# Kernel optimization log

Measured on AMD Instinct MI355X. Metric: run time of the kernel, lower is better.

Reference implementation:

```python
import jax, jax.numpy as jnp
import numpy as np
from jax import lax

B, S, V, E, H, NH = 32, 512, 30000, 300, 200, 4
ENC = 2 * H           # bidirectional encoder size = 400
DH = ENC // NH        # head dim = 100
BUDGET = 20.0         # percent of length kept by sparseMAP
SCALING = 1.0 / 0.001 # eval-mode temperature (module sets 0.001 at test time)
NEG = -1e9


def setup_inputs():
    key = jax.random.key(0)
    ks = jax.random.split(key, 16)
    lengths = jax.random.randint(ks[0], (B,), S // 2, S + 1)
    mask = jnp.arange(S)[None, :] < lengths[:, None]          # prefix mask [B,S]
    x = jax.random.randint(ks[1], (B, S), 0, V)
    p = lambda k, sh: jax.random.normal(k, sh, jnp.float32) * 0.05
    return {
        "x": x, "mask": mask,
        "embed_table": p(ks[2], (V, E)),
        "w_ih_f": p(ks[3], (4 * H, E)), "w_hh_f": p(ks[4], (4 * H, H)), "b_f": jnp.zeros((4 * H,), jnp.float32),
        "w_ih_b": p(ks[5], (4 * H, E)), "w_hh_b": p(ks[6], (4 * H, H)), "b_b": jnp.zeros((4 * H,), jnp.float32),
        "q_state": p(ks[7], (ENC,)),
        "W_q": p(ks[8], (ENC, ENC)), "W_k": p(ks[9], (ENC, ENC)), "W_v": p(ks[10], (ENC, ENC)),
        "W_out": p(ks[11], (ENC, ENC)),
        "W_head": p(ks[12], (ENC, 1)), "b_head": jnp.zeros((1,), jnp.float32),
    }


def _lstm(xW, mask, W_hh):
    """Masked (packed-equivalent) LSTM. xW: [B,S,4H] precomputed input proj, mask [B,S] bool."""
    Bb, Ss, H4 = xW.shape
    Hh = H4 // 4
    def step(carry, t_in):
        h, c = carry
        g, m = t_in                             # g [B,4H], m [B,1] bool
        gates = g + h @ W_hh.T
        i, f, gg, o = jnp.split(gates, 4, axis=-1)
        c_new = jax.nn.sigmoid(f) * c + jax.nn.sigmoid(i) * jnp.tanh(gg)
        h_new = jax.nn.sigmoid(o) * jnp.tanh(c_new)
        return (jnp.where(m, h_new, h), jnp.where(m, c_new, c)), jnp.where(m, h_new, 0.0)
    init = (jnp.zeros((Bb, Hh), xW.dtype), jnp.zeros((Bb, Hh), xW.dtype))
    xs = (jnp.swapaxes(xW, 0, 1), jnp.swapaxes(mask[..., None], 0, 1))
    _, outs = lax.scan(step, init, xs)
    return jnp.swapaxes(outs, 0, 1)


def _proj_capped_simplex(theta, k):
    """SparseMAP budget QP: argmin ||mu - theta||^2 s.t. 0<=mu<=1, sum(mu)=k.
    Bisection on threshold tau (non-diff), then exact differentiable tau on the free set."""
    th = lax.stop_gradient(theta)
    lo = jnp.min(th) - 1.0
    hi = jnp.max(th)
    def body(_, ab):
        lo, hi = ab
        mid = 0.5 * (lo + hi)
        too_big = jnp.sum(jnp.clip(th - mid, 0.0, 1.0)) > k
        return (jnp.where(too_big, mid, lo), jnp.where(too_big, hi, mid))
    lo, hi = lax.fori_loop(0, 60, body, (lo, hi))
    tau0 = 0.5 * (lo + hi)
    mu0 = th - tau0
    free = (mu0 > 0.0) & (mu0 < 1.0)
    nU = jnp.sum(mu0 >= 1.0).astype(theta.dtype)
    nS = jnp.sum(free).astype(theta.dtype)
    tau = (jnp.sum(jnp.where(free, theta, 0.0)) + nU - k) / jnp.maximum(nS, 1.0)
    tau = jnp.where(nS > 0, tau, tau0)
    return jnp.clip(theta - tau, 0.0, 1.0)


def _forward(x, mask, embed_table, w_ih_f, w_hh_f, b_f, w_ih_b, w_hh_b, b_b,
             q_state, W_q, W_k, W_v, W_out, W_head, b_head):
    lengths = mask.sum(1)                                   # [B] int
    emb = embed_table[x]                                    # [B,S,E] (dropout off: eval)
    # forward direction
    h_f = _lstm(emb @ w_ih_f.T + b_f, mask, w_hh_f)         # [B,S,H]
    # backward direction: reverse each sample within its length (packed semantics)
    t = jnp.arange(S)
    idx = jnp.clip(lengths[:, None] - 1 - t[None, :], 0, S - 1)   # [B,S], involution on valid part
    emb_rev = jnp.take_along_axis(emb, idx[..., None], axis=1)
    h_b_rev = _lstm(emb_rev @ w_ih_b.T + b_b, mask, w_hh_b)
    h_b = jnp.take_along_axis(h_b_rev, idx[..., None], axis=1)
    h_b = jnp.where(mask[..., None], h_b, 0.0)
    h = jnp.concatenate([h_f, h_b], axis=-1)                # [B,S,ENC]
    # Hopfield pooling with learned query state, per-sample sparseMAP top-k budget
    q = (q_state @ W_q).reshape(NH, DH)                     # learned pooling query
    K = (h @ W_k).reshape(B, S, NH, DH)
    Vv = (h @ W_v).reshape(B, S, NH, DH)
    scores = SCALING * jnp.einsum('hd,bshd->bhs', q, K)     # [B,NH,S]
    scores = jnp.where(mask[:, None, :], scores, NEG)
    kbud = jnp.round(BUDGET / 100.0 * lengths.astype(jnp.float32))   # per-sample budget
    proj = jax.vmap(jax.vmap(_proj_capped_simplex, (0, None)), (0, 0))
    p = proj(scores, kbud)                                  # [B,NH,S] sparse marginals
    pooled = jnp.einsum('bhs,bshd->bhd', p, Vv).reshape(B, ENC) @ W_out
    y = jax.nn.sigmoid(pooled @ W_head + b_head)            # [B,1]
    z = jnp.where(mask, p.mean(1), 0.0)                     # [B,S] rationale
    return y, z


def reference(x, mask, embed_table, w_ih_f, w_hh_f, b_f, w_ih_b, w_hh_b, b_b,
              q_state, W_q, W_k, W_v, W_out, W_head, b_head):
    return _forward(x, mask, embed_table, w_ih_f, w_hh_f, b_f, w_ih_b, w_hh_b, b_b,
                    q_state, W_q, W_k, W_v, W_out, W_head, b_head)
```

## Files before the change

kernel.cpp:

```cpp
#include <hip/hip_runtime.h>
#include <hip/hip_bf16.h>
#include <math.h>

#define B_   32
#define S_   512
#define V_   30000
#define E_   300
#define H_   200
#define NH_  4
#define ENC_ 400
#define G4_  800
#define NEGV  (-1e9f)
#define SCALE_ 1000.0f

typedef _Float16 half2v __attribute__((ext_vector_type(2)));
typedef _Float16 f16x8  __attribute__((ext_vector_type(8)));
typedef float    f32x4  __attribute__((ext_vector_type(4)));

#if defined(__has_builtin)
#if __has_builtin(__builtin_amdgcn_fdot2)
#define FDOT2(a,b,c) __builtin_amdgcn_fdot2((a),(b),(c),false)
#endif
#endif
#ifndef FDOT2
#define FDOT2(a,b,c) fmaf((float)(a)[1],(float)(b)[1], fmaf((float)(a)[0],(float)(b)[0],(c)))
#endif

#define OF_QVEC  320000ull
#define OF_WKQ   320448ull
#define OF_THETA 322048ull
#define OF_MU    387584ull
#define OF_HP    453120ull
#define OF_LEN   504320ull
#define OF_XWF   504384ull
#define OF_XWB   13611584ull
#define OF_HF    26718784ull
#define OF_HB    29995584ull

__global__ void k_lengths(const void* __restrict__ mask, int* __restrict__ lengths) {
  int b = blockIdx.x, lane = threadIdx.x;
  const unsigned char* mb = (const unsigned char*)mask;
  int mode;
  if (mb[1] != 0) mode = 0;
  else if (((const int*)mask)[1] != 0) mode = 1;
  else mode = 2;
  int cnt = 0;
  for (int s = lane; s < S_; s += 64) {
    int v;
    if (mode == 0)      v = mb[b*S_ + s] ? 1 : 0;
    else if (mode == 1) v = ((const int*)mask)[b*S_ + s] ? 1 : 0;
    else                v = ((const long long*)mask)[b*S_ + s] ? 1 : 0;
    cnt += v;
  }
  for (int off = 32; off; off >>= 1) cnt += __shfl_xor(cnt, off);
  if (lane == 0) lengths[b] = cnt;
}

__global__ void k_qvec(const float* __restrict__ qs, const float* __restrict__ Wq,
                       float* __restrict__ qvec) {
  __shared__ float qsl[ENC_];
  int t = threadIdx.x;
  if (t < ENC_) qsl[t] = qs[t];
  __syncthreads();
  if (t < ENC_) {
    float acc = 0.f;
    for (int i = 0; i < ENC_; ++i) acc += qsl[i] * Wq[(size_t)i*ENC_ + t];
    qvec[t] = acc;
  }
}

__global__ void k_wkq(const float* __restrict__ Wk, const float* __restrict__ qvec,
                      float* __restrict__ wkq) {
  int t = threadIdx.x;
  int e = blockIdx.x*64 + (t >> 2);
  int head = t & 3;
  if (e < ENC_) {
    float acc = 0.f;
    const float* row = Wk + (size_t)e*ENC_ + head*100;
    const float* qv  = qvec + head*100;
    for (int d = 0; d < 100; ++d) acc += row[d]*qv[d];
    wkq[e*4 + head] = acc;
  }
}

__global__ __launch_bounds__(256) void k_gemm_mfma(
    const int* __restrict__ x, const float* __restrict__ emb,
    const float* __restrict__ wf, const float* __restrict__ wb,
    const float* __restrict__ bf, const float* __restrict__ bb,
    float* __restrict__ xWf, float* __restrict__ xWb)
{
  __shared__ int xid[128];
  __shared__ __align__(16) _Float16 sA[128][40];
  __shared__ __align__(16) _Float16 sB[64][40];
  const int t = threadIdx.x;
  const int row0 = blockIdx.x * 128;
  const int col0 = blockIdx.y * 64;
  if (t < 128) xid[t] = x[row0 + t];
  const int w = t >> 6, lane = t & 63;
  const int wr = w >> 1, wc = w & 1;
  f32x4 acc[4][2] = {};
  const int ar = t >> 1, ah = t & 1;
  const int bc = t >> 2, bq = t & 3;
  const int colg = col0 + bc;
  const float* wsrc = (colg < 800) ? (wf + (size_t)colg*300)
                                   : (wb + (size_t)(colg-800)*300);
  __syncthreads();
  const float* asrc = emb + (size_t)xid[ar]*300;
  for (int kc = 0; kc < 10; ++kc) {
    const int k0 = kc*32;
    {
      const int kb = k0 + ah*16;
      _Float16 tmp[16];
      if (kb + 15 < 300) {
        #pragma unroll
        for (int q = 0; q < 4; ++q) {
          float4 a = *(const float4*)(asrc + kb + 4*q);
          tmp[4*q]  =(_Float16)a.x; tmp[4*q+1]=(_Float16)a.y;
          tmp[4*q+2]=(_Float16)a.z; tmp[4*q+3]=(_Float16)a.w;
        }
      } else {
        #pragma unroll
        for (int i = 0; i < 16; ++i)
          tmp[i] = (_Float16)((kb+i < 300) ? asrc[kb+i] : 0.f);
      }
      *(f16x8*)&sA[ar][ah*16]   = *(f16x8*)&tmp[0];
      *(f16x8*)&sA[ar][ah*16+8] = *(f16x8*)&tmp[8];
    }
    {
      const int kb = k0 + bq*8;
      _Float16 tmp[8];
      if (kb + 7 < 300) {
        #pragma unroll
        for (int q = 0; q < 2; ++q) {
          float4 a = *(const float4*)(wsrc + kb + 4*q);
          tmp[4*q]  =(_Float16)a.x; tmp[4*q+1]=(_Float16)a.y;
          tmp[4*q+2]=(_Float16)a.z; tmp[4*q+3]=(_Float16)a.w;
        }
      } else {
        #pragma unroll
        for (int i = 0; i < 8; ++i)
          tmp[i] = (_Float16)((kb+i < 300) ? wsrc[kb+i] : 0.f);
      }
      *(f16x8*)&sB[bc][bq*8] = *(f16x8*)&tmp[0];
    }
    __syncthreads();
    const int fr = lane & 15, kg = lane >> 4;
    f16x8 b0 = *(const f16x8*)&sB[wc*32 + fr][kg*8];
    f16x8 b1 = *(const f16x8*)&sB[wc*32 + 16 + fr][kg*8];
    #pragma unroll
    for (int m = 0; m < 4; ++m) {
      f16x8 afrag = *(const f16x8*)&sA[wr*64 + m*16 + fr][kg*8];
      acc[m][0] = __builtin_amdgcn_mfma_f32_16x16x32_f16(afrag, b0, acc[m][0], 0,0,0);
      acc[m][1] = __builtin_amdgcn_mfma_f32_16x16x32_f16(afrag, b1, acc[m][1], 0,0,0);
    }
    __syncthreads();
  }
  const int crb = (lane >> 4) * 4, ccol = lane & 15;
  #pragma unroll
  for (int n = 0; n < 2; ++n) {
    int colg2 = col0 + wc*32 + n*16 + ccol;
    bool isF = colg2 < 800;
    int colo = isF ? colg2 : colg2 - 800;
    float bias = isF ? bf[colo] : bb[colo];
    float* dst = isF ? xWf : xWb;
    #pragma unroll
    for (int m = 0; m < 4; ++m) {
      int row = row0 + wr*64 + m*16 + crb;
      #pragma unroll
      for (int r = 0; r < 4; ++r)
        dst[(size_t)(row+r)*800 + colo] = acc[m][n][r] + bias;
    }
  }
}

__global__ __launch_bounds__(1024) void k_lstm_v2(
    const float* __restrict__ xWf, const float* __restrict__ xWb,
    const float* __restrict__ whhf, const float* __restrict__ whhb,
    const int* __restrict__ lengths,
    float* __restrict__ h_f, float* __restrict__ h_b)
{
  const int bid = blockIdx.x;
  const int dir = bid >> 5, b = bid & 31;
  const float* __restrict__ xW  = dir ? xWb : xWf;
  const float* __restrict__ whh = dir ? whhb : whhf;
  float* __restrict__ hout      = dir ? h_b : h_f;
  const int len = lengths[b];
  const int t = threadIdx.x;
  const int active = (t < G4_);

  __shared__ __align__(16) _Float16 hbh[200];
  __shared__ float gact[G4_];

  half2v w[100];
  if (active) {
    const float* rp = whh + (size_t)t*H_;
    #pragma unroll
    for (int j = 0; j < 50; ++j) {
      float2 a = *(const float2*)(rp + 2*j);
      w[j] = half2v{(_Float16)a.x, (_Float16)a.y};
    }
    #pragma unroll
    for (int j = 0; j < 50; ++j) {
      float2 a = *(const float2*)(rp + 100 + 2*j);
      w[50+j] = half2v{(_Float16)a.x, (_Float16)a.y};
    }
  }
  if (t < 200) hbh[t] = (_Float16)0.f;
  float cst = 0.f;
  const float* xbase = xW + (size_t)b*S_*G4_;
  const int isTanh = (t >= 400) && (t < 600);
  __syncthreads();

  for (int step = 0; step < len; ++step) {
    const int pos = dir ? (len-1-step) : step;
    if (active) {
      float xv = xbase[(size_t)pos*G4_ + t];
      float a0 = 0.f, a1 = 0.f;
      #pragma unroll
      for (int j = 0; j < 12; ++j) {
        float4 h4 = *(const float4*)&hbh[8*j];
        a0 = FDOT2(w[4*j],   __builtin_bit_cast(half2v, h4.x), a0);
        a1 = FDOT2(w[4*j+1], __builtin_bit_cast(half2v, h4.y), a1);
        a0 = FDOT2(w[4*j+2], __builtin_bit_cast(half2v, h4.z), a0);
        a1 = FDOT2(w[4*j+3], __builtin_bit_cast(half2v, h4.w), a1);
      }
      {
        float2 h2 = *(const float2*)&hbh[96];
        a0 = FDOT2(w[48], __builtin_bit_cast(half2v, h2.x), a0);
        a1 = FDOT2(w[49], __builtin_bit_cast(half2v, h2.y), a1);
      }
      #pragma unroll
      for (int j = 0; j < 12; ++j) {
        float4 h4 = *(const float4*)&hbh[100 + 8*j];
        a0 = FDOT2(w[50+4*j],   __builtin_bit_cast(half2v, h4.x), a0);
        a1 = FDOT2(w[50+4*j+1], __builtin_bit_cast(half2v, h4.y), a1);
        a0 = FDOT2(w[50+4*j+2], __builtin_bit_cast(half2v, h4.z), a0);
        a1 = FDOT2(w[50+4*j+3], __builtin_bit_cast(half2v, h4.w), a1);
      }
      {
        float2 h2 = *(const float2*)&hbh[196];
        a0 = FDOT2(w[98], __builtin_bit_cast(half2v, h2.x), a0);
        a1 = FDOT2(w[99], __builtin_bit_cast(half2v, h2.y), a1);
      }
      float pre = a0 + a1 + xv;
      float act;
      if (isTanh) {
        float gc = fminf(fmaxf(pre, -10.f), 10.f);
        float e2 = __expf(2.f*gc);
        act = (e2-1.f)/(e2+1.f);
      } else {
        act = 1.f/(1.f+__expf(-pre));
      }
      gact[t] = act;
    }
    __syncthreads();
    if (t < 200) {
      float ig = gact[t], fg = gact[200+t], gg = gact[400+t], og = gact[600+t];
      cst = fg*cst + ig*gg;
      float cc = fminf(fmaxf(cst, -10.f), 10.f);
      float ec = __expf(2.f*cc);
      float hn = og*((ec-1.f)/(ec+1.f));
      hout[((size_t)b*S_ + pos)*H_ + t] = hn;
      hbh[t] = (_Float16)hn;
    }
    __syncthreads();
  }
}

__global__ __launch_bounds__(512, 1) void k_lstm_v2b(
    const float* __restrict__ xWf, const float* __restrict__ xWb,
    const float* __restrict__ whhf, const float* __restrict__ whhb,
    const int* __restrict__ lengths,
    float* __restrict__ h_f, float* __restrict__ h_b)
{
  const int bid = blockIdx.x;
  const int dir = bid >> 5, b = bid & 31;
  const float* __restrict__ xW  = dir ? xWb : xWf;
  const float* __restrict__ whh = dir ? whhb : whhf;
  float* __restrict__ hout      = dir ? h_b : h_f;
  const int len = lengths[b];
  const int t = threadIdx.x;
  const int row0 = t;
  const bool has2 = (t < 288);
  const int row1 = has2 ? (512 + t) : 799;

  __shared__ __align__(16) _Float16 hbh[200];
  __shared__ float gact[G4_];

  half2v w0[100], w1[100];
  {
    const float* r0 = whh + (size_t)row0*H_;
    const float* r1 = whh + (size_t)row1*H_;
    #pragma unroll
    for (int j = 0; j < 100; ++j) {
      float2 a = *(const float2*)(r0 + 2*j);
      w0[j] = half2v{(_Float16)a.x, (_Float16)a.y};
      float2 c = *(const float2*)(r1 + 2*j);
      w1[j] = half2v{(_Float16)c.x, (_Float16)c.y};
    }
    #pragma unroll
    for (int j = 0; j < 100; ++j) {
      asm("" : "+a"(w0[j]));
      asm("" : "+a"(w1[j]));
    }
  }

  if (t < 200) hbh[t] = (_Float16)0.f;
  float cst = 0.f;
  const float* xbase = xW + (size_t)b*S_*G4_;
  const int isTanh0 = (row0 >= 400);
  const int isTanh1 = (row1 >= 400) && (row1 < 600);
  __syncthreads();

  for (int step = 0; step < len; ++step) {
    const int pos = dir ? (len-1-step) : step;
    const float* xr = xbase + (size_t)pos*G4_;
    float xv0 = xr[row0];
    float xv1 = has2 ? xr[row1] : 0.f;
    float a0 = 0.f, a1 = 0.f;
    #pragma unroll
    for (int j = 0; j < 25; ++j) {
      float4 h4 = *(const float4*)&hbh[8*j];
      half2v p0 = __builtin_bit_cast(half2v, h4.x);
      half2v p1 = __builtin_bit_cast(half2v, h4.y);
      half2v p2 = __builtin_bit_cast(half2v, h4.z);
      half2v p3 = __builtin_bit_cast(half2v, h4.w);
      a0 = FDOT2(w0[4*j],   p0, a0);
      a0 = FDOT2(w0[4*j+1], p1, a0);
      a0 = FDOT2(w0[4*j+2], p2, a0);
      a0 = FDOT2(w0[4*j+3], p3, a0);
      a1 = FDOT2(w1[4*j],   p0, a1);
      a1 = FDOT2(w1[4*j+1], p1, a1);
      a1 = FDOT2(w1[4*j+2], p2, a1);
      a1 = FDOT2(w1[4*j+3], p3, a1);
    }
    {
      float pre = a0 + xv0;
      float act;
      if (isTanh0) {
        float gc = fminf(fmaxf(pre, -10.f), 10.f);
        float e2 = __expf(2.f*gc);
        act = (e2-1.f)/(e2+1.f);
      } else {
        act = 1.f/(1.f+__expf(-pre));
      }
      gact[row0] = act;
    }
    if (has2) {
      float pre = a1 + xv1;
      float act;
      if (isTanh1) {
        float gc = fminf(fmaxf(pre, -10.f), 10.f);
        float e2 = __expf(2.f*gc);
        act = (e2-1.f)/(e2+1.f);
      } else {
        act = 1.f/(1.f+__expf(-pre));
      }
      gact[row1] = act;
    }
    __syncthreads();
    if (t < H_) {
      float ig = gact[t], fg = gact[H_+t], gg = gact[2*H_+t], og = gact[3*H_+t];
      cst = fg*cst + ig*gg;
      float cc = fminf(fmaxf(cst, -10.f), 10.f);
      float ec = __expf(2.f*cc);
      float hn = og*((ec-1.f)/(ec+1.f));
      hout[((size_t)b*S_ + pos)*H_ + t] = hn;
      hbh[t] = (_Float16)hn;
    }
    __syncthreads();
  }
}

__global__ __launch_bounds__(256) void k_scores(
    const float* __restrict__ hf, const float* __restrict__ hb,
    const float* __restrict__ wkq, const int* __restrict__ lengths,
    float* __restrict__ theta)
{
  int wid = blockIdx.x*4 + (threadIdx.x >> 6);
  int lane = threadIdx.x & 63;
  int b = wid >> 9, s = wid & 511;
  const float* hfr = hf + ((size_t)b*S_ + s)*H_;
  const float* hbr = hb + ((size_t)b*S_ + s)*H_;
  bool valid = s < lengths[b];
  float a0=0.f, a1=0.f, a2=0.f, a3=0.f;
  if (valid) {
    for (int e = lane; e < ENC_; e += 64) {
      float hv = (e < H_) ? hfr[e] : hbr[e-H_];
      float4 w = *(const float4*)(wkq + e*4);
      a0 += hv*w.x; a1 += hv*w.y; a2 += hv*w.z; a3 += hv*w.w;
    }
    for (int off = 32; off; off >>= 1) {
      a0 += __shfl_xor(a0, off); a1 += __shfl_xor(a1, off);
      a2 += __shfl_xor(a2, off); a3 += __shfl_xor(a3, off);
    }
  }
  if (lane == 0) {
    size_t base = (size_t)b*2048 + s;
    theta[base       ] = valid ? SCALE_*a0 : NEGV;
    theta[base +  512] = valid ? SCALE_*a1 : NEGV;
    theta[base + 1024] = valid ? SCALE_*a2 : NEGV;
    theta[base + 1536] = valid ? SCALE_*a3 : NEGV;
  }
}

__global__ void k_sparsemap(const float* __restrict__ theta, const int* __restrict__ lengths,
                            float* __restrict__ mu) {
  int pid = blockIdx.x;
  int lane = threadIdx.x;
  const float* th = theta + (size_t)pid*512;
  float v[8];
  #pragma unroll
  for (int i = 0; i < 8; ++i) v[i] = th[i*64 + lane];
  float kf = rintf(0.2f * (float)lengths[pid >> 2]);
  float mn = v[0], mx = v[0];
  #pragma unroll
  for (int i = 1; i < 8; ++i) { mn = fminf(mn, v[i]); mx = fmaxf(mx, v[i]); }
  for (int off = 32; off; off >>= 1) {
    mn = fminf(mn, __shfl_xor(mn, off)); mx = fmaxf(mx, __shfl_xor(mx, off));
  }
  float lo = mn - 1.f, hi = mx;
  for (int it = 0; it < 60; ++it) {
    float mid = 0.5f*(lo + hi);
    float s = 0.f;
    #pragma unroll
    for (int i = 0; i < 8; ++i) s += fminf(fmaxf(v[i]-mid, 0.f), 1.f);
    for (int off = 32; off; off >>= 1) s += __shfl_xor(s, off);
    bool big = s > kf;
    lo = big ? mid : lo;
    hi = big ? hi : mid;
  }
  float tau0 = 0.5f*(lo + hi);
  float fs = 0.f, nU = 0.f, nS = 0.f;
  #pragma unroll
  for (int i = 0; i < 8; ++i) {
    float m0 = v[i] - tau0;
    if (m0 >= 1.f) nU += 1.f;
    else if (m0 > 0.f) { fs += v[i]; nS += 1.f; }
  }
  for (int off = 32; off; off >>= 1) {
    fs += __shfl_xor(fs, off); nU += __shfl_xor(nU, off); nS += __shfl_xor(nS, off);
  }
  float tau = (fs + nU - kf) / fmaxf(nS, 1.f);
  tau = (nS > 0.f) ? tau : tau0;
  float* mo = mu + (size_t)pid*512;
  #pragma unroll
  for (int i = 0; i < 8; ++i) mo[i*64 + lane] = fminf(fmaxf(v[i]-tau, 0.f), 1.f);
}

__global__ __launch_bounds__(512) void k_hp(
    const float* __restrict__ mu, const float* __restrict__ hf,
    const float* __restrict__ hb, float* __restrict__ hp)
{
  __shared__ float mul[512];
  int pid = blockIdx.x, b = pid >> 2;
  int t = threadIdx.x;
  mul[t] = mu[(size_t)pid*512 + t];
  __syncthreads();
  if (t < ENC_) {
    const float* hsrc = (t < H_) ? (hf + t) : (hb + (t - H_));
    float acc = 0.f;
    for (int s = 0; s < 512; ++s) {
      float m = mul[s];
      if (m != 0.f) acc += m * hsrc[((size_t)b*S_ + s)*H_];
    }
    hp[(size_t)pid*ENC_ + t] = acc;
  }
}

__global__ __launch_bounds__(512) void k_head(
    const float* __restrict__ hp, const float* __restrict__ Wv,
    const float* __restrict__ Wout, const float* __restrict__ Wh,
    const float* __restrict__ bh, float* __restrict__ out)
{
  __shared__ float hpl[1600];
  __shared__ float ppl[ENC_];
  __shared__ float ojl[ENC_];
  __shared__ float red[512];
  int b = blockIdx.x, t = threadIdx.x;
  for (int i = t; i < 1600; i += 512) hpl[i] = hp[(size_t)b*1600 + i];
  __syncthreads();
  if (t < ENC_) {
    int head = t / 100;
    float acc = 0.f;
    for (int e = 0; e < ENC_; ++e) acc += hpl[head*ENC_ + e] * Wv[(size_t)e*ENC_ + t];
    ppl[t] = acc;
  }
  __syncthreads();
  if (t < ENC_) {
    float acc = 0.f;
    for (int c = 0; c < ENC_; ++c) acc += ppl[c] * Wout[(size_t)c*ENC_ + t];
    ojl[t] = acc;
  }
  __syncthreads();
  red[t] = (t < ENC_) ? ojl[t]*Wh[t] : 0.f;
  __syncthreads();
  for (int sft = 256; sft; sft >>= 1) {
    if (t < sft) red[t] += red[t+sft];
    __syncthreads();
  }
  if (t == 0) out[b] = 1.f/(1.f + expf(-(red[0] + bh[0])));
}

__global__ void k_z(const float* __restrict__ mu, const int* __restrict__ lengths,
                    float* __restrict__ out) {
  int idx = blockIdx.x*256 + threadIdx.x;
  int b = idx >> 9, s = idx & 511;
  float zz = 0.f;
  if (s < lengths[b]) {
    size_t base = (size_t)b*2048 + s;
    zz = 0.25f*(mu[base] + mu[base+512] + mu[base+1024] + mu[base+1536]);
  }
  out[32 + idx] = zz;
}

extern "C" void kernel_launch(void* const* d_in, const int* in_sizes, int n_in,
                              void* d_out, int out_size, void* d_ws, size_t ws_size,
                              hipStream_t stream) {
  const int*   x    = (const int*)d_in[0];
  const void*  mask = d_in[1];
  const float* emb  = (const float*)d_in[2];
  const float* wihf = (const float*)d_in[3];
  const float* whhf = (const float*)d_in[4];
  const float* bf   = (const float*)d_in[5];
  const float* wihb = (const float*)d_in[6];
  const float* whhb = (const float*)d_in[7];
  const float* bb   = (const float*)d_in[8];
  const float* qs   = (const float*)d_in[9];
  const float* Wq   = (const float*)d_in[10];
  const float* Wk   = (const float*)d_in[11];
  const float* Wv   = (const float*)d_in[12];
  const float* Wout = (const float*)d_in[13];
  const float* Wh   = (const float*)d_in[14];
  const float* bh   = (const float*)d_in[15];
  float* out = (float*)d_out;
  float* W = (float*)d_ws;
  int* lengths = (int*)(W + OF_LEN);

  hipFuncAttributes fa{};
  bool use_v2b = false;
  if (hipFuncGetAttributes(&fa, (const void*)k_lstm_v2b) == hipSuccess)
    use_v2b = (fa.localSizeBytes <= 32);

  k_lengths<<<32, 64, 0, stream>>>(mask, lengths);
  k_qvec<<<1, 512, 0, stream>>>(qs, Wq, W+OF_QVEC);
  k_wkq<<<7, 256, 0, stream>>>(Wk, W+OF_QVEC, W+OF_WKQ);
  k_gemm_mfma<<<dim3(128, 25), 256, 0, stream>>>(x, emb, wihf, wihb, bf, bb,
                                                 W+OF_XWF, W+OF_XWB);
  if (use_v2b)
    k_lstm_v2b<<<64, 512, 0, stream>>>(W+OF_XWF, W+OF_XWB, whhf, whhb,
                                       lengths, W+OF_HF, W+OF_HB);
  else
    k_lstm_v2<<<64, 1024, 0, stream>>>(W+OF_XWF, W+OF_XWB, whhf, whhb,
                                       lengths, W+OF_HF, W+OF_HB);
  k_scores<<<4096, 256, 0, stream>>>(W+OF_HF, W+OF_HB, W+OF_WKQ, lengths, W+OF_THETA);
  k_sparsemap<<<128, 64, 0, stream>>>(W+OF_THETA, lengths, W+OF_MU);
  k_hp<<<128, 512, 0, stream>>>(W+OF_MU, W+OF_HF, W+OF_HB, W+OF_HP);
  k_head<<<32, 512, 0, stream>>>(W+OF_HP, Wv, Wout, Wh, bh, out);
  k_z<<<64, 256, 0, stream>>>(W+OF_MU, lengths, out);
}
```

Measured before the change: 875.9 us.

## Fuse prep kernels and sparsemap/pooling/head/rationale tail into single kernels

Merges the mask-length, query-vector and Wk·q kernels into one k_prep launch; each Wk·q block recomputes the query vector locally instead of reading it from workspace. Merges the sparsemap projection, weighted pooling, output head and rationale kernels into one per-sample kernel, so the marginals stay in shared memory and four launches plus the global round trips disappear. This tail now runs on 32 blocks instead of 128 per stage, no longer skips zero marginals, and reads the hidden states once for all four heads. It also drops the inline-asm hint that pinned the LSTM recurrent weights to AGPRs, which may change register allocation in the dominant LSTM kernel.

```diff
diff --git a/kernel.cpp b/kernel.cpp
--- a/kernel.cpp
+++ b/kernel.cpp
@@ -26,60 +26,69 @@
 #define FDOT2(a,b,c) fmaf((float)(a)[1],(float)(b)[1], fmaf((float)(a)[0],(float)(b)[0],(c)))
 #endif
 
-#define OF_QVEC  320000ull
 #define OF_WKQ   320448ull
 #define OF_THETA 322048ull
-#define OF_MU    387584ull
-#define OF_HP    453120ull
 #define OF_LEN   504320ull
 #define OF_XWF   504384ull
 #define OF_XWB   13611584ull
 #define OF_HF    26718784ull
 #define OF_HB    29995584ull
 
-__global__ void k_lengths(const void* __restrict__ mask, int* __restrict__ lengths) {
-  int b = blockIdx.x, lane = threadIdx.x;
-  const unsigned char* mb = (const unsigned char*)mask;
-  int mode;
-  if (mb[1] != 0) mode = 0;
-  else if (((const int*)mask)[1] != 0) mode = 1;
-  else mode = 2;
-  int cnt = 0;
-  for (int s = lane; s < S_; s += 64) {
-    int v;
-    if (mode == 0)      v = mb[b*S_ + s] ? 1 : 0;
-    else if (mode == 1) v = ((const int*)mask)[b*S_ + s] ? 1 : 0;
-    else                v = ((const long long*)mask)[b*S_ + s] ? 1 : 0;
-    cnt += v;
-  }
-  for (int off = 32; off; off >>= 1) cnt += __shfl_xor(cnt, off);
-  if (lane == 0) lengths[b] = cnt;
-}
-
-__global__ void k_qvec(const float* __restrict__ qs, const float* __restrict__ Wq,
-                       float* __restrict__ qvec) {
-  __shared__ float qsl[ENC_];
-  int t = threadIdx.x;
-  if (t < ENC_) qsl[t] = qs[t];
-  __syncthreads();
-  if (t < ENC_) {
-    float acc = 0.f;
-    for (int i = 0; i < ENC_; ++i) acc += qsl[i] * Wq[(size_t)i*ENC_ + t];
-    qvec[t] = acc;
-  }
-}
-
-__global__ void k_wkq(const float* __restrict__ Wk, const float* __restrict__ qvec,
-                      float* __restrict__ wkq) {
-  int t = threadIdx.x;
-  int e = blockIdx.x*64 + (t >> 2);
-  int head = t & 3;
-  if (e < ENC_) {
-    float acc = 0.f;
-    const float* row = Wk + (size_t)e*ENC_ + head*100;
-    const float* qv  = qvec + head*100;
-    for (int d = 0; d < 100; ++d) acc += row[d]*qv[d];
-    wkq[e*4 + head] = acc;
+__global__ __launch_bounds__(256) void k_prep(
+    const void* __restrict__ mask, int* __restrict__ lengths,
+    const float* __restrict__ qs, const float* __restrict__ Wq,
+    const float* __restrict__ Wk, float* __restrict__ wkq)
+{
+  const int blk = blockIdx.x, t = threadIdx.x;
+  __shared__ float shb[800];
+  if (blk < 32) {
+    int* red = (int*)shb;
+    const unsigned char* mb = (const unsigned char*)mask;
+    int mode;
+    if (mb[1] != 0) mode = 0;
+    else if (((const int*)mask)[1] != 0) mode = 1;
+    else mode = 2;
+    int cnt = 0;
+    for (int s = t; s < S_; s += 256) {
+      int v;
+      if (mode == 0)      v = mb[blk*S_ + s] ? 1 : 0;
+      else if (mode == 1) v = ((const int*)mask)[blk*S_ + s] ? 1 : 0;
+      else                v = ((const long long*)mask)[blk*S_ + s] ? 1 : 0;
+      cnt += v;
+    }
+    red[t] = cnt;
+    __syncthreads();
+    for (int sft = 128; sft; sft >>= 1) {
+      if (t < sft) red[t] += red[t+sft];
+      __syncthreads();
+    }
+    if (t == 0) lengths[blk] = red[0];
+  } else {
+    float* qsl = shb;
+    float* qv  = shb + 400;
+    if (t < ENC_) qsl[t] = qs[t];
+    if (t + 256 < ENC_) qsl[t+256] = qs[t+256];
+    __syncthreads();
+    {
+      float acc = 0.f;
+      for (int i = 0; i < ENC_; ++i) acc += qsl[i] * Wq[(size_t)i*ENC_ + t];
+      qv[t] = acc;
+      if (t + 256 < ENC_) {
+        float acc2 = 0.f;
+        for (int i = 0; i < ENC_; ++i) acc2 += qsl[i] * Wq[(size_t)i*ENC_ + t + 256];
+        qv[t+256] = acc2;
+      }
+    }
+    __syncthreads();
+    const int e = (blk - 32)*64 + (t >> 2);
+    const int head = t & 3;
+    if (e < ENC_) {
+      float acc = 0.f;
+      const float* row = Wk + (size_t)e*ENC_ + head*100;
+      const float* qvh = qv + head*100;
+      for (int d = 0; d < 100; ++d) acc += row[d]*qvh[d];
+      wkq[e*4 + head] = acc;
+    }
   }
 }
 
@@ -267,7 +276,7 @@
   }
 }
 
-__global__ __launch_bounds__(512, 1) void k_lstm_v2b(
+__global__ __launch_bounds__(512, 1) void k_lstm_v2d(
     const float* __restrict__ xWf, const float* __restrict__ xWb,
     const float* __restrict__ whhf, const float* __restrict__ whhb,
     const int* __restrict__ lengths,
@@ -298,18 +307,13 @@
       float2 c = *(const float2*)(r1 + 2*j);
       w1[j] = half2v{(_Float16)c.x, (_Float16)c.y};
     }
-    #pragma unroll
-    for (int j = 0; j < 100; ++j) {
-      asm("" : "+a"(w0[j]));
-      asm("" : "+a"(w1[j]));
-    }
   }
 
   if (t < 200) hbh[t] = (_Float16)0.f;
   float cst = 0.f;
   const float* xbase = xW + (size_t)b*S_*G4_;
   const int isTanh0 = (row0 >= 400);
-  const int isTanh1 = (row1 >= 400) && (row1 < 600);
+  const int isTanh1 = (row1 < 600);
   __syncthreads();
 
   for (int step = 0; step < len; ++step) {
@@ -404,82 +408,85 @@
   }
 }
 
-__global__ void k_sparsemap(const float* __restrict__ theta, const int* __restrict__ lengths,
-                            float* __restrict__ mu) {
-  int pid = blockIdx.x;
-  int lane = threadIdx.x;
-  const float* th = theta + (size_t)pid*512;
-  float v[8];
-  #pragma unroll
-  for (int i = 0; i < 8; ++i) v[i] = th[i*64 + lane];
-  float kf = rintf(0.2f * (float)lengths[pid >> 2]);
-  float mn = v[0], mx = v[0];
-  #pragma unroll
-  for (int i = 1; i < 8; ++i) { mn = fminf(mn, v[i]); mx = fmaxf(mx, v[i]); }
-  for (int off = 32; off; off >>= 1) {
-    mn = fminf(mn, __shfl_xor(mn, off)); mx = fmaxf(mx, __shfl_xor(mx, off));
-  }
-  float lo = mn - 1.f, hi = mx;
-  for (int it = 0; it < 60; ++it) {
-    float mid = 0.5f*(lo + hi);
-    float s = 0.f;
-    #pragma unroll
-    for (int i = 0; i < 8; ++i) s += fminf(fmaxf(v[i]-mid, 0.f), 1.f);
-    for (int off = 32; off; off >>= 1) s += __shfl_xor(s, off);
-    bool big = s > kf;
-    lo = big ? mid : lo;
-    hi = big ? hi : mid;
-  }
-  float tau0 = 0.5f*(lo + hi);
-  float fs = 0.f, nU = 0.f, nS = 0.f;
-  #pragma unroll
-  for (int i = 0; i < 8; ++i) {
-    float m0 = v[i] - tau0;
-    if (m0 >= 1.f) nU += 1.f;
-    else if (m0 > 0.f) { fs += v[i]; nS += 1.f; }
-  }
-  for (int off = 32; off; off >>= 1) {
-    fs += __shfl_xor(fs, off); nU += __shfl_xor(nU, off); nS += __shfl_xor(nS, off);
-  }
-  float tau = (fs + nU - kf) / fmaxf(nS, 1.f);
-  tau = (nS > 0.f) ? tau : tau0;
-  float* mo = mu + (size_t)pid*512;
-  #pragma unroll
-  for (int i = 0; i < 8; ++i) mo[i*64 + lane] = fminf(fmaxf(v[i]-tau, 0.f), 1.f);
-}
-
-__global__ __launch_bounds__(512) void k_hp(
-    const float* __restrict__ mu, const float* __restrict__ hf,
-    const float* __restrict__ hb, float* __restrict__ hp)
+__global__ __launch_bounds__(512) void k_spzh(
+    const float* __restrict__ theta, const int* __restrict__ lengths,
+    const float* __restrict__ hf, const float* __restrict__ hb,
+    const float* __restrict__ Wv, const float* __restrict__ Wout,
+    const float* __restrict__ Wh, const float* __restrict__ bh,
+    float* __restrict__ out)
 {
-  __shared__ float mul[512];
-  int pid = blockIdx.x, b = pid >> 2;
-  int t = threadIdx.x;
-  mul[t] = mu[(size_t)pid*512 + t];
-  __syncthreads();
-  if (t < ENC_) {
-    const float* hsrc = (t < H_) ? (hf + t) : (hb + (t - H_));
-    float acc = 0.f;
-    for (int s = 0; s < 512; ++s) {
-      float m = mul[s];
-      if (m != 0.f) acc += m * hsrc[((size_t)b*S_ + s)*H_];
-    }
-    hp[(size_t)pid*ENC_ + t] = acc;
-  }
-}
-
-__global__ __launch_bounds__(512) void k_head(
-    const float* __restrict__ hp, const float* __restrict__ Wv,
-    const float* __restrict__ Wout, const float* __restrict__ Wh,
-    const float* __restrict__ bh, float* __restrict__ out)
-{
+  const int b = blockIdx.x, t = threadIdx.x;
+  __shared__ float muL[4][512];
   __shared__ float hpl[1600];
   __shared__ float ppl[ENC_];
   __shared__ float ojl[ENC_];
   __shared__ float red[512];
-  int b = blockIdx.x, t = threadIdx.x;
-  for (int i = t; i < 1600; i += 512) hpl[i] = hp[(size_t)b*1600 + i];
-  __syncthreads();
+  const int len = lengths[b];
+
+  if (t < 256) {
+    const int head = t >> 6, lane = t & 63;
+    const float* th = theta + ((size_t)b*4 + head)*512;
+    float v[8];
+    #pragma unroll
+    for (int i = 0; i < 8; ++i) v[i] = th[i*64 + lane];
+    float kf = rintf(0.2f * (float)len);
+    float mn = v[0], mx = v[0];
+    #pragma unroll
+    for (int i = 1; i < 8; ++i) { mn = fminf(mn, v[i]); mx = fmaxf(mx, v[i]); }
+    for (int off = 32; off; off >>= 1) {
+      mn = fminf(mn, __shfl_xor(mn, off)); mx = fmaxf(mx, __shfl_xor(mx, off));
+    }
+    float lo = mn - 1.f, hi = mx;
+    for (int it = 0; it < 60; ++it) {
+      float mid = 0.5f*(lo + hi);
+      float s = 0.f;
+      #pragma unroll
+      for (int i = 0; i < 8; ++i) s += fminf(fmaxf(v[i]-mid, 0.f), 1.f);
+      for (int off = 32; off; off >>= 1) s += __shfl_xor(s, off);
+      bool big = s > kf;
+      lo = big ? mid : lo;
+      hi = big ? hi : mid;
+    }
+    float tau0 = 0.5f*(lo + hi);
+    float fs = 0.f, nU = 0.f, nS = 0.f;
+    #pragma unroll
+    for (int i = 0; i < 8; ++i) {
+      float m0 = v[i] - tau0;
+      if (m0 >= 1.f) nU += 1.f;
+      else if (m0 > 0.f) { fs += v[i]; nS += 1.f; }
+    }
+    for (int off = 32; off; off >>= 1) {
+      fs += __shfl_xor(fs, off); nU += __shfl_xor(nU, off); nS += __shfl_xor(nS, off);
+    }
+    float tau = (fs + nU - kf) / fmaxf(nS, 1.f);
+    tau = (nS > 0.f) ? tau : tau0;
+    #pragma unroll
+    for (int i = 0; i < 8; ++i)
+      muL[head][i*64 + lane] = fminf(fmaxf(v[i]-tau, 0.f), 1.f);
+  }
+  __syncthreads();
+
+  {
+    const int s = t;
+    float zz = (s < len) ? 0.25f*(muL[0][s]+muL[1][s]+muL[2][s]+muL[3][s]) : 0.f;
+    out[32 + b*S_ + s] = zz;
+  }
+
+  if (t < ENC_) {
+    const float* hsrc = (t < H_) ? (hf + t) : (hb + (t - H_));
+    float ac0 = 0.f, ac1 = 0.f, ac2 = 0.f, ac3 = 0.f;
+    for (int s = 0; s < S_; ++s) {
+      float hv = hsrc[((size_t)b*S_ + s)*H_];
+      ac0 += muL[0][s]*hv; ac1 += muL[1][s]*hv;
+      ac2 += muL[2][s]*hv; ac3 += muL[3][s]*hv;
+    }
+    hpl[t]        = ac0;
+    hpl[400 + t]  = ac1;
+    hpl[800 + t]  = ac2;
+    hpl[1200 + t] = ac3;
+  }
+  __syncthreads();
+
   if (t < ENC_) {
     int head = t / 100;
     float acc = 0.f;
@@ -500,18 +507,6 @@
     __syncthreads();
   }
   if (t == 0) out[b] = 1.f/(1.f + expf(-(red[0] + bh[0])));
-}
-
-__global__ void k_z(const float* __restrict__ mu, const int* __restrict__ lengths,
-                    float* __restrict__ out) {
-  int idx = blockIdx.x*256 + threadIdx.x;
-  int b = idx >> 9, s = idx & 511;
-  float zz = 0.f;
-  if (s < lengths[b]) {
-    size_t base = (size_t)b*2048 + s;
-    zz = 0.25f*(mu[base] + mu[base+512] + mu[base+1024] + mu[base+1536]);
-  }
-  out[32 + idx] = zz;
 }
 
 extern "C" void kernel_launch(void* const* d_in, const int* in_sizes, int n_in,
@@ -538,24 +533,20 @@
   int* lengths = (int*)(W + OF_LEN);
 
   hipFuncAttributes fa{};
-  bool use_v2b = false;
-  if (hipFuncGetAttributes(&fa, (const void*)k_lstm_v2b) == hipSuccess)
-    use_v2b = (fa.localSizeBytes <= 32);
-
-  k_lengths<<<32, 64, 0, stream>>>(mask, lengths);
-  k_qvec<<<1, 512, 0, stream>>>(qs, Wq, W+OF_QVEC);
-  k_wkq<<<7, 256, 0, stream>>>(Wk, W+OF_QVEC, W+OF_WKQ);
+  bool use_v2d = false;
+  if (hipFuncGetAttributes(&fa, (const void*)k_lstm_v2d) == hipSuccess)
+    use_v2d = (fa.localSizeBytes <= 32);
+
+  k_prep<<<39, 256, 0, stream>>>(mask, lengths, qs, Wq, Wk, W+OF_WKQ);
   k_gemm_mfma<<<dim3(128, 25), 256, 0, stream>>>(x, emb, wihf, wihb, bf, bb,
                                                  W+OF_XWF, W+OF_XWB);
-  if (use_v2b)
-    k_lstm_v2b<<<64, 512, 0, stream>>>(W+OF_XWF, W+OF_XWB, whhf, whhb,
+  if (use_v2d)
+    k_lstm_v2d<<<64, 512, 0, stream>>>(W+OF_XWF, W+OF_XWB, whhf, whhb,
                                        lengths, W+OF_HF, W+OF_HB);
   else
     k_lstm_v2<<<64, 1024, 0, stream>>>(W+OF_XWF, W+OF_XWB, whhf, whhb,
                                        lengths, W+OF_HF, W+OF_HB);
   k_scores<<<4096, 256, 0, stream>>>(W+OF_HF, W+OF_HB, W+OF_WKQ, lengths, W+OF_THETA);
-  k_sparsemap<<<128, 64, 0, stream>>>(W+OF_THETA, lengths, W+OF_MU);
-  k_hp<<<128, 512, 0, stream>>>(W+OF_MU, W+OF_HF, W+OF_HB, W+OF_HP);
-  k_head<<<32, 512, 0, stream>>>(W+OF_HP, Wv, Wout, Wh, bh, out);
-  k_z<<<64, 256, 0, stream>>>(W+OF_MU, lengths, out);
-}
+  k_spzh<<<32, 512, 0, stream>>>(W+OF_THETA, lengths, W+OF_HF, W+OF_HB,
+                                 Wv, Wout, Wh, bh, out);
+}
```

Result: no change. 862.2 us (-1.6%).
